# Optimization experiments

Hardware: AMD Instinct MI355X
Metric: run time of the kernel (lower is better)

The kernel has to match this reference:

```python
import jax, jax.numpy as jnp
import numpy as np

NUM_HEADS = 16
HEAD_DIM = 64  # d_model // num_heads = 1024 // 16
NUM_BUCKETS = 20


def setup_inputs() -> dict:
    key = jax.random.key(0)
    ks = jax.random.split(key, 5)
    B, S, D = 2, 2048, 1024
    v = jax.random.normal(ks[0], (B, S, D), dtype=jnp.float32)
    k = jax.random.normal(ks[1], (B, S, D), dtype=jnp.float32)
    q = jax.random.normal(ks[2], (B, S, D), dtype=jnp.float32)
    mask = jax.random.randint(ks[3], (B, S, S), 0, 2).astype(jnp.bool_)
    diff_matrix = jax.random.randint(ks[4], (B, S, S), 0, NUM_BUCKETS)
    rel_bias = jax.random.normal(jax.random.fold_in(key, 7), (NUM_BUCKETS, NUM_HEADS), dtype=jnp.float32)
    return {"v": v, "k": k, "q": q, "mask": mask, "diff_matrix": diff_matrix, "rel_bias": rel_bias}


def _split_heads(x):
    B, S, _ = x.shape
    return x.reshape(B, S, NUM_HEADS, HEAD_DIM).transpose(0, 2, 1, 3)  # [B,H,S,hd]


def reference(v, k, q, mask, diff_matrix, rel_bias):
    B, S, D = q.shape
    qh, kh, vh = _split_heads(q), _split_heads(k), _split_heads(v)
    scale = 1.0 / jnp.sqrt(jnp.float32(HEAD_DIM))
    scores = jnp.einsum('bhqd,bhkd->bhqk', qh, kh) * scale  # [B,H,S,S]
    # relative bias: gather [B,S,S,H] -> [B,H,S,S]
    bias = rel_bias[diff_matrix].transpose(0, 3, 1, 2)
    att = jax.nn.silu(scores + bias)
    att = jnp.where(mask[:, None, :, :], att, 0.0)
    av = jnp.einsum('bhqk,bhkd->bhqd', att, vh)  # [B,H,S,hd]
    return av.transpose(0, 2, 1, 3).reshape(B, S, D)
```

## Files before the change

kernel.cpp:

```cpp
#include <hip/hip_runtime.h>
#include <hip/hip_fp16.h>
#include <cstdint>
#include <cstddef>

#define SEQ 2048
#define DM 1024
#define NH 16
#define NB 20

typedef _Float16 half8 __attribute__((ext_vector_type(8)));
typedef _Float16 half4 __attribute__((ext_vector_type(4)));
typedef _Float16 h2v __attribute__((ext_vector_type(2)));
typedef float f32x4 __attribute__((ext_vector_type(4)));
typedef float f32x2 __attribute__((ext_vector_type(2)));
typedef int i32x4 __attribute__((ext_vector_type(4)));
typedef unsigned int u32;
typedef unsigned int u32x2 __attribute__((ext_vector_type(2)));

#define KF_HALVES 4194304
#define VF_HALVES 4194304

__global__ __launch_bounds__(256) void pa_prep(
    const float* __restrict__ v, const float* __restrict__ k,
    const int* __restrict__ diff, const int* __restrict__ mask,
    _Float16* __restrict__ KF, _Float16* __restrict__ VF,
    unsigned char* __restrict__ PB) {
  const int bid = blockIdx.x, tid = threadIdx.x;
  if (bid < 2048) {
    int img = bid >> 4;
    int bb = img >> 6, kt = img & 63;
    int tix = ((bid & 15) << 8) | tid;
    int r = tix >> 7;
    int c0 = (tix & 127) << 3;
    const float* src = k + ((size_t)(bb * SEQ + kt * 32 + r)) * DM + c0;
    f32x4 a = *(const f32x4*)src;
    f32x4 c = *(const f32x4*)(src + 4);
    half8 o = {(_Float16)a[0], (_Float16)a[1], (_Float16)a[2], (_Float16)a[3],
               (_Float16)c[0], (_Float16)c[1], (_Float16)c[2], (_Float16)c[3]};
    int h = c0 >> 6, dh = (c0 >> 5) & 1, g4 = (c0 >> 3) & 3;
    int k2 = r >> 4, l16 = r & 15;
    int lane = g4 * 16 + l16;
    size_t off = ((size_t)((bb * 16 + h) * 64 + kt)) * 2048 + (k2 * 2 + dh) * 512 + lane * 8;
    *(half8*)(KF + off) = o;
  } else if (bid < 3072) {
    int b3 = bid - 2048;
    int img = b3 >> 3;
    int bb = img >> 6, kt = img & 63;
    int tix = ((b3 & 7) << 8) | tid;
    int kq = tix >> 8;
    int k2 = kq >> 2, g4 = kq & 3;
    int d0 = (tix & 255) << 2;
    const float* src = v + ((size_t)(bb * SEQ + kt * 32 + k2 * 16 + g4 * 4)) * DM + d0;
    f32x4 m0 = *(const f32x4*)(src);
    f32x4 m1 = *(const f32x4*)(src + DM);
    f32x4 m2 = *(const f32x4*)(src + 2 * DM);
    f32x4 m3 = *(const f32x4*)(src + 3 * DM);
#pragma unroll
    for (int i = 0; i < 4; ++i) {
      int d = d0 + i;
      int l16 = d & 15, dt = (d >> 4) & 3, h = d >> 6;
      int lane = g4 * 16 + l16;
      half4 o = {(_Float16)m0[i], (_Float16)m1[i], (_Float16)m2[i], (_Float16)m3[i]};
      size_t off = ((size_t)((bb * 16 + h) * 64 + kt)) * 2048 + dt * 512 + lane * 8 + k2 * 4;
      *(half4*)(VF + off) = o;
    }
  } else {
    int b4 = bid - 3072;
    int job = b4 >> 5;
    int bb = job >> 6, qblk = job & 63;
    int tix = ((b4 & 31) << 8) | tid;
    int kt = tix >> 7;
    int rem = tix & 127;
    int g4 = rem & 3, l16 = (rem >> 2) & 15, qs = rem >> 6;
    int lane = g4 * 16 + l16;
    int qrow = qblk * 32 + qs * 16 + l16;
    size_t rowbase = ((size_t)(bb * SEQ + qrow)) * SEQ;
    u32x2 wds;
#pragma unroll
    for (int k2 = 0; k2 < 2; ++k2) {
      int kk = kt * 32 + k2 * 16 + g4 * 4;
      i32x4 dv = *(const i32x4*)(diff + rowbase + kk);
      i32x4 mv = *(const i32x4*)(mask + rowbase + kk);
      u32 bk[4];
#pragma unroll
      for (int r = 0; r < 4; ++r) bk[r] = mv[r] ? (u32)dv[r] : 20u;
      u32 pi01 = bk[0] * 21 + bk[1];
      u32 pi23 = bk[2] * 21 + bk[3];
      wds[k2] = pi01 | (pi23 << 16);
    }
    size_t off = ((size_t)job) * 65536 + (size_t)kt * 1024 + (size_t)lane * 16 + (size_t)qs * 8;
    *(u32x2*)(PB + off) = wds;
  }
}

__device__ __forceinline__ void gll16(const _Float16* g, _Float16* l) {
  __builtin_amdgcn_global_load_lds(
      (const __attribute__((address_space(1))) unsigned int*)g,
      (__attribute__((address_space(3))) unsigned int*)l, 16, 0, 0);
}

__device__ __forceinline__ half4 silu4nb(const f32x4& s) {
  h2v x01 = __builtin_bit_cast(h2v, __builtin_amdgcn_cvt_pkrtz(s[0], s[1]));
  h2v x23 = __builtin_bit_cast(h2v, __builtin_amdgcn_cvt_pkrtz(s[2], s[3]));
  const h2v NL2E = {(_Float16)-1.44269504f, (_Float16)-1.44269504f};
  const h2v ONE = {(_Float16)1.0f, (_Float16)1.0f};
  h2v m01 = x01 * NL2E, m23 = x23 * NL2E;
  h2v e01 = __builtin_bit_cast(h2v, h2exp2(__builtin_bit_cast(__half2, m01)));
  h2v e23 = __builtin_bit_cast(h2v, h2exp2(__builtin_bit_cast(__half2, m23)));
  h2v d01 = e01 + ONE, d23 = e23 + ONE;
  h2v y01 = x01 * __builtin_bit_cast(h2v, h2rcp(__builtin_bit_cast(__half2, d01)));
  h2v y23 = x23 * __builtin_bit_cast(h2v, h2rcp(__builtin_bit_cast(__half2, d23)));
  return (half4){y01[0], y01[1], y23[0], y23[1]};
}

struct BiasSet { f32x4 b[2][2]; };

__global__ __launch_bounds__(256, 4) void pa_main(
    const _Float16* __restrict__ KF, const _Float16* __restrict__ VF,
    const unsigned char* __restrict__ PB, const float* __restrict__ q,
    const float* __restrict__ relbias, float* __restrict__ out) {
  __shared__ _Float16 ringK[2][2048];
  __shared__ f32x2 tabF[441];

  const int tid = threadIdx.x, lane = tid & 63, wid = tid >> 6;
  const int l16 = lane & 15, g4 = lane >> 4;
  const int xcd = blockIdx.x & 7;
  const int i = blockIdx.x >> 3;
  const int b = xcd >> 2;
  const int hg = xcd & 3;
  const int h = hg * 4 + (i & 3);
  const int qgrp = i >> 2;
  const int qblk = qgrp * 4 + wid;
  const int qbase = qblk * 32;

  for (int e = tid; e < 441; e += 256) {
    int bi = e / 21, bj = e - bi * 21;
    float vi = (bi < NB) ? relbias[bi * NH + h] : -30000.0f;
    float vj = (bj < NB) ? relbias[bj * NH + h] : -30000.0f;
    tabF[e] = (f32x2){vi, vj};
  }

  half8 qf[2][2];
#pragma unroll
  for (int qs = 0; qs < 2; ++qs)
#pragma unroll
    for (int dh = 0; dh < 2; ++dh) {
      const float* s = q + ((size_t)(b * SEQ + qbase + qs * 16 + l16)) * DM + h * 64 + dh * 32 + g4 * 8;
      f32x4 a = *(const f32x4*)s;
      f32x4 c = *(const f32x4*)(s + 4);
      qf[qs][dh] = {(_Float16)(a[0] * 0.125f), (_Float16)(a[1] * 0.125f),
                    (_Float16)(a[2] * 0.125f), (_Float16)(a[3] * 0.125f),
                    (_Float16)(c[0] * 0.125f), (_Float16)(c[1] * 0.125f),
                    (_Float16)(c[2] * 0.125f), (_Float16)(c[3] * 0.125f)};
    }

  f32x4 acc[2][4];
#pragma unroll
  for (int qs = 0; qs < 2; ++qs)
#pragma unroll
    for (int dt = 0; dt < 4; ++dt) acc[qs][dt] = (f32x4){0.f, 0.f, 0.f, 0.f};

  const _Float16* kfb = KF + ((size_t)((b * 16 + h) * 64)) * 2048 + lane * 8;
  const _Float16* vfb = VF + ((size_t)((b * 16 + h) * 64)) * 2048 + lane * 8;
  const unsigned char* pbb = PB + ((size_t)(b * 64 + qblk)) * 65536 + lane * 16;
  const int c512 = wid * 512;

#define STAGE(T, B) gll16(kfb + (size_t)(T) * 2048 + c512, &ringK[B][c512])
#define CLMP(T) ((T) < 64 ? (T) : 63)

#define GATHER(BS, PQ)                                                 \
  do {                                                                 \
    _Pragma("unroll") for (int qs = 0; qs < 2; ++qs)                   \
      _Pragma("unroll") for (int k2 = 0; k2 < 2; ++k2) {               \
        u32 w = (u32)PQ[qs * 2 + k2];                                  \
        f32x2 p01 = tabF[w & 0xffffu];                                 \
        f32x2 p23 = tabF[w >> 16];                                     \
        BS.b[qs][k2] = (f32x4){p01[0], p01[1], p23[0], p23[1]};        \
      }                                                                \
  } while (0)

#define COMPUTE(B, BS, T)                                                                    \
  do {                                                                                       \
    half8 vvr[4];                                                                            \
    _Pragma("unroll") for (int j = 0; j < 4; ++j)                                            \
      vvr[j] = *(const half8*)(vfb + (size_t)(T) * 2048 + j * 512);     \
    half8 kfr[4];                                                                            \
    _Pragma("unroll") for (int j = 0; j < 4; ++j)                                            \
      kfr[j] = *(const half8*)&ringK[B][j * 512 + lane * 8];                   \
    f32x4 sa[2][2];                                                                          \
    _Pragma("unroll") for (int qs = 0; qs < 2; ++qs)                                         \
      _Pragma("unroll") for (int k2 = 0; k2 < 2; ++k2) {                                     \
        sa[qs][k2] = __builtin_amdgcn_mfma_f32_16x16x32_f16(kfr[k2 * 2 + 0], qf[qs][0],      \
                                                            BS.b[qs][k2], 0, 0, 0);          \
        sa[qs][k2] = __builtin_amdgcn_mfma_f32_16x16x32_f16(kfr[k2 * 2 + 1], qf[qs][1],      \
                                                            sa[qs][k2], 0, 0, 0);            \
      }                                                                                      \
    half8 pf8[2];                                                                            \
    _Pragma("unroll") for (int qs = 0; qs < 2; ++qs) {                                       \
      half4 p0 = silu4nb(sa[qs][0]);                                                         \
      half4 p1 = silu4nb(sa[qs][1]);                                                         \
      pf8[qs] = (half8){p0[0], p0[1], p0[2], p0[3], p1[0], p1[1], p1[2], p1[3]};             \
    }                                                                                        \
    _Pragma("unroll") for (int qs = 0; qs < 2; ++qs)                                         \
      _Pragma("unroll") for (int dt = 0; dt < 4; ++dt)                                       \
        acc[qs][dt] = __builtin_amdgcn_mfma_f32_16x16x32_f16(pf8[qs], vvr[dt],               \
                                                             acc[qs][dt], 0, 0, 0);          \
  } while (0)

  BiasSet biasA, biasB;
  i32x4 pq1, pqX;

  STAGE(0, 0);
  i32x4 pq0 = *(const i32x4*)(pbb);
  pq1 = *(const i32x4*)(pbb + 1024);
  __syncthreads();
  GATHER(biasA, pq0);

  for (int t = 0; t < 64; t += 2) {
    STAGE(t + 1, 1);
    pqX = *(const i32x4*)(pbb + (size_t)CLMP(t + 2) * 1024);
    __builtin_amdgcn_sched_barrier(0);
    GATHER(biasB, pq1);
    COMPUTE(0, biasA, t);
    __syncthreads();
    STAGE(CLMP(t + 2), 0);
    pq1 = *(const i32x4*)(pbb + (size_t)CLMP(t + 3) * 1024);
    __builtin_amdgcn_sched_barrier(0);
    GATHER(biasA, pqX);
    COMPUTE(1, biasB, t + 1);
    __syncthreads();
  }
#undef STAGE
#undef CLMP
#undef GATHER
#undef COMPUTE

#pragma unroll
  for (int qs = 0; qs < 2; ++qs)
#pragma unroll
    for (int dt = 0; dt < 4; ++dt)
#pragma unroll
      for (int r = 0; r < 4; ++r) {
        int qrow = qbase + qs * 16 + g4 * 4 + r;
        int d = h * 64 + dt * 16 + l16;
        out[((size_t)(b * SEQ) + qrow) * DM + d] = acc[qs][dt][r];
      }
}

extern "C" void kernel_launch(void* const* d_in, const int* in_sizes, int n_in,
                              void* d_out, int out_size, void* d_ws, size_t ws_size,
                              hipStream_t stream) {
  const float* v = (const float*)d_in[0];
  const float* k = (const float*)d_in[1];
  const float* q = (const float*)d_in[2];
  const int* mask = (const int*)d_in[3];
  const int* diff = (const int*)d_in[4];
  const float* relbias = (const float*)d_in[5];
  float* out = (float*)d_out;

  _Float16* KF = (_Float16*)d_ws;
  _Float16* VF = KF + KF_HALVES;
  unsigned char* PB = (unsigned char*)(VF + VF_HALVES);
  if (ws_size < (size_t)25165824) return;

  pa_prep<<<7168, 256, 0, stream>>>(v, k, diff, mask, KF, VF, PB);
  pa_main<<<512, 256, 0, stream>>>(KF, VF, PB, q, relbias, out);
}
```

Baseline: 91.35 us.

## Split key loop across two wave groups per block with shared-memory reduction

Blocks grow from 256 to 512 threads. The second group of four waves processes the odd key tiles for the same query blocks, while the first group takes the even ones. The K ring buffer grows to four slots, and each parity group stages its own tiles. Partial accumulators are combined through LDS at the end. The aim is more waves and latency hiding per query block, at the cost of extra barriers per iteration, a final reduction, and higher register/LDS pressure under launch bounds of 512x4.

```diff
diff --git a/kernel.cpp b/kernel.cpp
--- a/kernel.cpp
+++ b/kernel.cpp
@@ -115,14 +115,15 @@
 
 struct BiasSet { f32x4 b[2][2]; };
 
-__global__ __launch_bounds__(256, 4) void pa_main(
+__global__ __launch_bounds__(512, 4) void pa_main(
     const _Float16* __restrict__ KF, const _Float16* __restrict__ VF,
     const unsigned char* __restrict__ PB, const float* __restrict__ q,
     const float* __restrict__ relbias, float* __restrict__ out) {
-  __shared__ _Float16 ringK[2][2048];
+  __shared__ __align__(16) _Float16 ringK[4][2048];
   __shared__ f32x2 tabF[441];
 
   const int tid = threadIdx.x, lane = tid & 63, wid = tid >> 6;
+  const int w4 = wid & 3, par = wid >> 2;
   const int l16 = lane & 15, g4 = lane >> 4;
   const int xcd = blockIdx.x & 7;
   const int i = blockIdx.x >> 3;
@@ -130,10 +131,10 @@
   const int hg = xcd & 3;
   const int h = hg * 4 + (i & 3);
   const int qgrp = i >> 2;
-  const int qblk = qgrp * 4 + wid;
+  const int qblk = qgrp * 4 + w4;
   const int qbase = qblk * 32;
 
-  for (int e = tid; e < 441; e += 256) {
+  for (int e = tid; e < 441; e += 512) {
     int bi = e / 21, bj = e - bi * 21;
     float vi = (bi < NB) ? relbias[bi * NH + h] : -30000.0f;
     float vj = (bj < NB) ? relbias[bj * NH + h] : -30000.0f;
@@ -163,9 +164,9 @@
   const _Float16* kfb = KF + ((size_t)((b * 16 + h) * 64)) * 2048 + lane * 8;
   const _Float16* vfb = VF + ((size_t)((b * 16 + h) * 64)) * 2048 + lane * 8;
   const unsigned char* pbb = PB + ((size_t)(b * 64 + qblk)) * 65536 + lane * 16;
-  const int c512 = wid * 512;
-
-#define STAGE(T, B) gll16(kfb + (size_t)(T) * 2048 + c512, &ringK[B][c512])
+  const int c512 = w4 * 512;
+
+#define STAGE(T) gll16(kfb + (size_t)(T) * 2048 + c512, &ringK[(T) & 3][c512])
 #define CLMP(T) ((T) < 64 ? (T) : 63)
 
 #define GATHER(BS, PQ)                                                 \
@@ -179,14 +180,15 @@
       }                                                                \
   } while (0)
 
-#define COMPUTE(B, BS, T)                                                                    \
+#define COMPUTE(T, BS)                                                                       \
   do {                                                                                       \
+    int sl_ = (T) & 3;                                                                       \
     half8 vvr[4];                                                                            \
     _Pragma("unroll") for (int j = 0; j < 4; ++j)                                            \
-      vvr[j] = *(const half8*)(vfb + (size_t)(T) * 2048 + j * 512);     \
+      vvr[j] = *(const half8*)(vfb + (size_t)(T) * 2048 + j * 512);           \
     half8 kfr[4];                                                                            \
     _Pragma("unroll") for (int j = 0; j < 4; ++j)                                            \
-      kfr[j] = *(const half8*)&ringK[B][j * 512 + lane * 8];                   \
+      kfr[j] = *(const half8*)&ringK[sl_][j * 512 + lane * 8];                 \
     f32x4 sa[2][2];                                                                          \
     _Pragma("unroll") for (int qs = 0; qs < 2; ++qs)                                         \
       _Pragma("unroll") for (int k2 = 0; k2 < 2; ++k2) {                                     \
@@ -207,27 +209,23 @@
                                                              acc[qs][dt], 0, 0, 0);          \
   } while (0)
 
-  BiasSet biasA, biasB;
-  i32x4 pq1, pqX;
-
-  STAGE(0, 0);
-  i32x4 pq0 = *(const i32x4*)(pbb);
-  pq1 = *(const i32x4*)(pbb + 1024);
+  BiasSet bias;
+  i32x4 pqCur, pqNext;
+
+  STAGE(par);
+  STAGE(par + 2);
+  pqCur = *(const i32x4*)(pbb + (size_t)par * 1024);
   __syncthreads();
-  GATHER(biasA, pq0);
-
-  for (int t = 0; t < 64; t += 2) {
-    STAGE(t + 1, 1);
-    pqX = *(const i32x4*)(pbb + (size_t)CLMP(t + 2) * 1024);
+
+  for (int p = 0; p < 32; ++p) {
+    const int T = 2 * p + par;
+    pqNext = *(const i32x4*)(pbb + (size_t)CLMP(T + 2) * 1024);
     __builtin_amdgcn_sched_barrier(0);
-    GATHER(biasB, pq1);
-    COMPUTE(0, biasA, t);
-    __syncthreads();
-    STAGE(CLMP(t + 2), 0);
-    pq1 = *(const i32x4*)(pbb + (size_t)CLMP(t + 3) * 1024);
-    __builtin_amdgcn_sched_barrier(0);
-    GATHER(biasA, pqX);
-    COMPUTE(1, biasB, t + 1);
+    GATHER(bias, pqCur);
+    COMPUTE(T, bias);
+    __syncthreads();
+    if (T + 4 < 64) STAGE(T + 4);
+    pqCur = pqNext;
     __syncthreads();
   }
 #undef STAGE
@@ -235,16 +233,28 @@
 #undef GATHER
 #undef COMPUTE
 
-#pragma unroll
-  for (int qs = 0; qs < 2; ++qs)
-#pragma unroll
-    for (int dt = 0; dt < 4; ++dt)
-#pragma unroll
-      for (int r = 0; r < 4; ++r) {
-        int qrow = qbase + qs * 16 + g4 * 4 + r;
-        int d = h * 64 + dt * 16 + l16;
-        out[((size_t)(b * SEQ) + qrow) * DM + d] = acc[qs][dt][r];
+  f32x4* red = (f32x4*)ringK;
+#pragma unroll
+  for (int qs = 0; qs < 2; ++qs) {
+    __syncthreads();
+    if (par == 1) {
+#pragma unroll
+      for (int dt = 0; dt < 4; ++dt) red[(w4 * 64 + lane) * 4 + dt] = acc[qs][dt];
+    }
+    __syncthreads();
+    if (par == 0) {
+#pragma unroll
+      for (int dt = 0; dt < 4; ++dt) {
+        f32x4 sum = acc[qs][dt] + red[(w4 * 64 + lane) * 4 + dt];
+#pragma unroll
+        for (int r = 0; r < 4; ++r) {
+          int qrow = qbase + qs * 16 + g4 * 4 + r;
+          int d = h * 64 + dt * 16 + l16;
+          out[((size_t)(b * SEQ) + qrow) * DM + d] = sum[r];
+        }
       }
+    }
+  }
 }
 
 extern "C" void kernel_launch(void* const* d_in, const int* in_sizes, int n_in,
@@ -264,5 +274,5 @@
   if (ws_size < (size_t)25165824) return;
 
   pa_prep<<<7168, 256, 0, stream>>>(v, k, diff, mask, KF, VF, PB);
-  pa_main<<<512, 256, 0, stream>>>(KF, VF, PB, q, relbias, out);
-}
+  pa_main<<<512, 512, 0, stream>>>(KF, VF, PB, q, relbias, out);
+}
```

After: 87.30 us (median of 2 runs). 4.4% less time.
